# Kernel tuning notes

Measured on AMD Instinct MI355X. Metric: run time of the kernel, lower is better.

Reference implementation:

```python
import jax, jax.numpy as jnp
import numpy as np

B, N, GN, GS = 16, 100000, 4096, 64  # batch, points, num_groups, group_size


def setup_inputs() -> dict:
    key = jax.random.key(0)
    k1, k2, k3 = jax.random.split(key, 3)
    x_proto = jax.random.normal(k1, (B, N, 3), dtype=jnp.float32)
    template = jax.random.normal(k2, (N, 3), dtype=jnp.float32)
    groups = jax.random.randint(k3, (GN, GS), 0, N, dtype=jnp.int32)
    return {"x_proto": x_proto, "template": template, "groups": groups}


def reference(x_proto, template, groups):
    # x_proto: [B, N, 3], template: [N, 3], groups: [GN, GS] int indices
    b, n, _ = x_proto.shape
    Yg = template[groups]                      # [GN, GS, 3] gathered template
    Xg = x_proto[:, groups]                    # [B, GN, GS, 3] gathered current points

    # Kabsch: align template group Y to current X (R @ Y + t ~ X)
    muY = Yg.mean(axis=1)                      # [GN, 3]
    muX = Xg.mean(axis=2)                      # [B, GN, 3]
    Yc = Yg - muY[:, None, :]
    Xc = Xg - muX[:, :, None, :]
    H = jnp.einsum('gni,bgnj->bgij', Yc, Xc)   # [B, GN, 3, 3] covariance
    U, S, Vh = jnp.linalg.svd(H)
    V = jnp.swapaxes(Vh, -2, -1)
    R0 = V @ jnp.swapaxes(U, -2, -1)
    det = jnp.linalg.det(R0)                   # [B, GN]
    # flip last column of V where det < 0 to get a proper rotation
    s = jnp.where(det < 0, -1.0, 1.0).astype(x_proto.dtype)
    col_scale = jnp.stack([jnp.ones_like(s), jnp.ones_like(s), s], axis=-1)  # [B, GN, 3]
    R = (V * col_scale[..., None, :]) @ jnp.swapaxes(U, -2, -1)              # [B, GN, 3, 3]
    t = muX - jnp.einsum('bgij,gj->bgi', R, muY)                             # [B, GN, 3]

    # project template group through (R, t)
    Xg_proj = jnp.einsum('bgij,gnj->bgni', R, Yg) + t[:, :, None, :]         # [B, GN, GS, 3]

    # scatter-add with overlap counting, then average
    flat_idx = groups.reshape(-1)              # [GN*GS]
    out = jnp.zeros_like(x_proto).at[:, flat_idx].add(Xg_proj.reshape(b, -1, 3))
    counts = jnp.zeros((n,), dtype=x_proto.dtype).at[flat_idx].add(1.0)
    counts = jnp.maximum(counts, 1.0)
    return out / counts[None, :, None]
```

## Files before the change

### kernel.cpp

```cpp
#include <hip/hip_runtime.h>
#include <math.h>

static constexpr int BB = 16;
static constexpr int NN = 100000;
static constexpr int GN = 4096;
static constexpr int GS = 64;
static constexpr int NP = BB * GN;
static constexpr int NE = GN * GS;
static constexpr int NBLK = (NN + 255) / 256;

__device__ __forceinline__ float wsum64(float v) {
#pragma unroll
  for (int off = 32; off > 0; off >>= 1) v += __shfl_xor(v, off, 64);
  return v;
}

__global__ __launch_bounds__(256) void k_zero(int4* __restrict__ cnt4) {
  int t = blockIdx.x * 256 + threadIdx.x;
  if (t < NN / 4) cnt4[t] = make_int4(0, 0, 0, 0);
}

__global__ __launch_bounds__(256) void k_tpl(
    const float* __restrict__ tpl, const int* __restrict__ groups,
    float* __restrict__ Yg, float* __restrict__ GmY, int* __restrict__ cnt) {
  int g    = blockIdx.x * 4 + (threadIdx.x >> 6);
  int lane = threadIdx.x & 63;
  int idx = groups[g * GS + lane];
  atomicAdd(&cnt[idx], 1);
  float y0 = tpl[idx * 3 + 0], y1 = tpl[idx * 3 + 1], y2 = tpl[idx * 3 + 2];
  float* o = Yg + ((size_t)g * GS + lane) * 3;
  o[0] = y0; o[1] = y1; o[2] = y2;
  float sy0 = wsum64(y0), sy1 = wsum64(y1), sy2 = wsum64(y2);
  if (lane == 0) {
    const float inv = 1.0f / 64.0f;
    float4 m = make_float4(sy0 * inv, sy1 * inv, sy2 * inv, 0.0f);
    *(float4*)(GmY + (size_t)g * 4) = m;
  }
}

__global__ __launch_bounds__(256) void k_stats(
    const float* __restrict__ x, const float* __restrict__ Yg,
    const float* __restrict__ GmY, const int* __restrict__ groups,
    float* __restrict__ Ht) {
  int wid4 = blockIdx.x * 4 + (threadIdx.x >> 6);
  int lane = threadIdx.x & 63;
  int s    = lane >> 4;
  int l4   = lane & 15;
  int p = wid4 * 4 + s;
  int b = p >> 12;
  int g = p & (GN - 1);

  int4 iv = *(const int4*)(groups + (size_t)g * GS + l4 * 4);
  const float4* yv = (const float4*)(Yg + ((size_t)g * GS + l4 * 4) * 3);
  float4 ya = yv[0], yb = yv[1], yc = yv[2];

  const float* xb = x + (size_t)b * NN * 3;
  float sx0 = 0.f, sx1 = 0.f, sx2 = 0.f;
  float h00 = 0.f, h01 = 0.f, h02 = 0.f;
  float h10 = 0.f, h11 = 0.f, h12 = 0.f;
  float h20 = 0.f, h21 = 0.f, h22 = 0.f;

#define ACC(Y0, Y1, Y2, IDX)                                   \
  {                                                            \
    const float* xp = xb + (size_t)(IDX) * 3;                  \
    float x0 = xp[0], x1 = xp[1], x2 = xp[2];                  \
    sx0 += x0; sx1 += x1; sx2 += x2;                           \
    h00 += (Y0) * x0; h01 += (Y0) * x1; h02 += (Y0) * x2;      \
    h10 += (Y1) * x0; h11 += (Y1) * x1; h12 += (Y1) * x2;      \
    h20 += (Y2) * x0; h21 += (Y2) * x1; h22 += (Y2) * x2;      \
  }
  ACC(ya.x, ya.y, ya.z, iv.x);
  ACC(ya.w, yb.x, yb.y, iv.y);
  ACC(yb.z, yb.w, yc.x, iv.z);
  ACC(yc.y, yc.z, yc.w, iv.w);
#undef ACC

#define RED(V)                                                 \
  V += __shfl_xor(V, 8, 64); V += __shfl_xor(V, 4, 64);        \
  V += __shfl_xor(V, 2, 64); V += __shfl_xor(V, 1, 64);
  RED(sx0) RED(sx1) RED(sx2)
  RED(h00) RED(h01) RED(h02)
  RED(h10) RED(h11) RED(h12)
  RED(h20) RED(h21) RED(h22)
#undef RED

  if (l4 == 0) {
    const float inv = 1.0f / 64.0f;
    float4 m = *(const float4*)(GmY + (size_t)g * 4);
    float mx0 = sx0 * inv, mx1 = sx1 * inv, mx2 = sx2 * inv;
    float4 o0 = make_float4(mx0, mx1, mx2, h00 - m.x * sx0);
    float4 o1 = make_float4(h01 - m.x * sx1, h02 - m.x * sx2,
                            h10 - m.y * sx0, h11 - m.y * sx1);
    float4 o2 = make_float4(h12 - m.y * sx2, h20 - m.z * sx0,
                            h21 - m.z * sx1, h22 - m.z * sx2);
    float* o = Ht + (size_t)p * 12;
    *(float4*)(o + 0) = o0;
    *(float4*)(o + 4) = o1;
    *(float4*)(o + 8) = o2;
  }
}

#define JROT(P, Q, RR)                                                        \
  {                                                                           \
    float apq = K[P][Q];                                                      \
    if (fabsf(apq) > 1e-30f) {                                                \
      float app = K[P][P], aqq = K[Q][Q];                                     \
      float tau = (aqq - app) / (2.0f * apq);                                 \
      float tt = copysignf(1.0f, tau) / (fabsf(tau) + sqrtf(1.0f + tau*tau)); \
      float cc = 1.0f / sqrtf(1.0f + tt * tt);                                \
      float ss = tt * cc;                                                     \
      K[P][P] = app - tt * apq;                                               \
      K[Q][Q] = aqq + tt * apq;                                               \
      K[P][Q] = 0.0f; K[Q][P] = 0.0f;                                         \
      float krp = K[RR][P], krq = K[RR][Q];                                   \
      K[RR][P] = cc * krp - ss * krq; K[P][RR] = K[RR][P];                    \
      K[RR][Q] = ss * krp + cc * krq; K[Q][RR] = K[RR][Q];                    \
      float v0p = V[0][P], v0q = V[0][Q];                                     \
      float v1p = V[1][P], v1q = V[1][Q];                                     \
      float v2p = V[2][P], v2q = V[2][Q];                                     \
      V[0][P] = cc * v0p - ss * v0q; V[0][Q] = ss * v0p + cc * v0q;           \
      V[1][P] = cc * v1p - ss * v1q; V[1][Q] = ss * v1p + cc * v1q;           \
      V[2][P] = cc * v2p - ss * v2q; V[2][Q] = ss * v2p + cc * v2q;           \
    }                                                                         \
  }

#define FIN(AA, BBi, CC)                                                      \
  {                                                                           \
    float va0 = V[0][AA], va1 = V[1][AA], va2 = V[2][AA];                     \
    float vb0 = V[0][BBi], vb1 = V[1][BBi], vb2 = V[2][BBi];                  \
    float vc0 = V[0][CC], vc1 = V[1][CC], vc2 = V[2][CC];                     \
    float ua0 = A[0][0]*va0 + A[0][1]*va1 + A[0][2]*va2;                      \
    float ua1 = A[1][0]*va0 + A[1][1]*va1 + A[1][2]*va2;                      \
    float ua2 = A[2][0]*va0 + A[2][1]*va1 + A[2][2]*va2;                      \
    float il = 1.0f / sqrtf(ua0*ua0 + ua1*ua1 + ua2*ua2 + 1e-30f);            \
    ua0 *= il; ua1 *= il; ua2 *= il;                                          \
    float ub0 = A[0][0]*vb0 + A[0][1]*vb1 + A[0][2]*vb2;                      \
    float ub1 = A[1][0]*vb0 + A[1][1]*vb1 + A[1][2]*vb2;                      \
    float ub2 = A[2][0]*vb0 + A[2][1]*vb1 + A[2][2]*vb2;                      \
    il = 1.0f / sqrtf(ub0*ub0 + ub1*ub1 + ub2*ub2 + 1e-30f);                  \
    ub0 *= il; ub1 *= il; ub2 *= il;                                          \
    float dd = ua0*ub0 + ua1*ub1 + ua2*ub2;                                   \
    ub0 -= dd * ua0; ub1 -= dd * ua1; ub2 -= dd * ua2;                        \
    il = 1.0f / sqrtf(ub0*ub0 + ub1*ub1 + ub2*ub2 + 1e-30f);                  \
    ub0 *= il; ub1 *= il; ub2 *= il;                                          \
    float uc0 = ua1*ub2 - ua2*ub1;                                            \
    float uc1 = ua2*ub0 - ua0*ub2;                                            \
    float uc2 = ua0*ub1 - ua1*ub0;                                            \
    R[0][0] = va0*ua0 + vb0*ub0 + dsg*vc0*uc0;                                \
    R[0][1] = va0*ua1 + vb0*ub1 + dsg*vc0*uc1;                                \
    R[0][2] = va0*ua2 + vb0*ub2 + dsg*vc0*uc2;                                \
    R[1][0] = va1*ua0 + vb1*ub0 + dsg*vc1*uc0;                                \
    R[1][1] = va1*ua1 + vb1*ub1 + dsg*vc1*uc1;                                \
    R[1][2] = va1*ua2 + vb1*ub2 + dsg*vc1*uc2;                                \
    R[2][0] = va2*ua0 + vb2*ub0 + dsg*vc2*uc0;                                \
    R[2][1] = va2*ua1 + vb2*ub1 + dsg*vc2*uc1;                                \
    R[2][2] = va2*ua2 + vb2*ub2 + dsg*vc2*uc2;                                \
  }

__global__ __launch_bounds__(256) void k_svd(
    const float* __restrict__ Ht, const float* __restrict__ GmY,
    float* __restrict__ Rt) {
  int p = blockIdx.x * 256 + threadIdx.x;
  if (p >= NP) return;
  int g = p & (GN - 1);
  const float* h = Ht + (size_t)p * 12;
  float4 f0 = *(const float4*)(h + 0);
  float4 f1 = *(const float4*)(h + 4);
  float4 f2 = *(const float4*)(h + 8);
  float4 m  = *(const float4*)(GmY + (size_t)g * 4);
  float mx0 = f0.x, mx1 = f0.y, mx2 = f0.z;
  float my0 = m.x, my1 = m.y, my2 = m.z;
  float A[3][3];
  A[0][0] = f0.w; A[0][1] = f1.x; A[0][2] = f1.y;
  A[1][0] = f1.z; A[1][1] = f1.w; A[1][2] = f2.x;
  A[2][0] = f2.y; A[2][1] = f2.z; A[2][2] = f2.w;

  float K[3][3];
#pragma unroll
  for (int i = 0; i < 3; ++i)
#pragma unroll
    for (int j = 0; j < 3; ++j)
      K[i][j] = A[0][i]*A[0][j] + A[1][i]*A[1][j] + A[2][i]*A[2][j];

  float V[3][3] = {{1.f,0.f,0.f},{0.f,1.f,0.f},{0.f,0.f,1.f}};
#pragma unroll
  for (int sweep = 0; sweep < 5; ++sweep) {
    JROT(0, 1, 2);
    JROT(0, 2, 1);
    JROT(1, 2, 0);
  }

  float d0 = K[0][0], d1 = K[1][1], d2 = K[2][2];
  float detV = V[0][0]*(V[1][1]*V[2][2] - V[1][2]*V[2][1])
             - V[0][1]*(V[1][0]*V[2][2] - V[1][2]*V[2][0])
             + V[0][2]*(V[1][0]*V[2][1] - V[1][1]*V[2][0]);
  float dsg = (detV < 0.0f) ? -1.0f : 1.0f;

  float R[3][3];
  if (d0 <= d1 && d0 <= d2) {
    FIN(1, 2, 0);
  } else if (d1 <= d0 && d1 <= d2) {
    FIN(2, 0, 1);
  } else {
    FIN(0, 1, 2);
  }

  float t0 = mx0 - (R[0][0]*my0 + R[0][1]*my1 + R[0][2]*my2);
  float t1 = mx1 - (R[1][0]*my0 + R[1][1]*my1 + R[1][2]*my2);
  float t2 = mx2 - (R[2][0]*my0 + R[2][1]*my1 + R[2][2]*my2);

  float* o = Rt + (size_t)p * 12;
  o[0] = R[0][0]; o[1] = R[0][1]; o[2] = R[0][2];
  o[3] = R[1][0]; o[4] = R[1][1]; o[5] = R[1][2];
  o[6] = R[2][0]; o[7] = R[2][1]; o[8] = R[2][2];
  o[9] = t0; o[10] = t1; o[11] = t2;
}

__global__ __launch_bounds__(256) void k_scan1(
    const int* __restrict__ cnt, int* __restrict__ blockSums) {
  __shared__ int lds[4];
  int t = blockIdx.x * 256 + threadIdx.x;
  int v = (t < NN) ? cnt[t] : 0;
#pragma unroll
  for (int off = 32; off > 0; off >>= 1) v += __shfl_xor(v, off, 64);
  if ((threadIdx.x & 63) == 0) lds[threadIdx.x >> 6] = v;
  __syncthreads();
  if (threadIdx.x == 0)
    blockSums[blockIdx.x] = lds[0] + lds[1] + lds[2] + lds[3];
}

__global__ __launch_bounds__(512) void k_scan2(int* __restrict__ blockSums) {
  __shared__ int lds[512];
  int tid = threadIdx.x;
  int v = (tid < NBLK) ? blockSums[tid] : 0;
  lds[tid] = v;
  __syncthreads();
#pragma unroll
  for (int off = 1; off < 512; off <<= 1) {
    int add = (tid >= off) ? lds[tid - off] : 0;
    __syncthreads();
    lds[tid] += add;
    __syncthreads();
  }
  if (tid < NBLK) blockSums[tid] = lds[tid] - v;
}

__global__ __launch_bounds__(256) void k_scan3(
    const int* __restrict__ cnt, const int* __restrict__ blockSums,
    int* __restrict__ row_start, int* __restrict__ cursor) {
  __shared__ int lds[256];
  int tid = threadIdx.x;
  int t = blockIdx.x * 256 + tid;
  int v = (t < NN) ? cnt[t] : 0;
  lds[tid] = v;
  __syncthreads();
#pragma unroll
  for (int off = 1; off < 256; off <<= 1) {
    int add = (tid >= off) ? lds[tid - off] : 0;
    __syncthreads();
    lds[tid] += add;
    __syncthreads();
  }
  if (t < NN) {
    row_start[t] = lds[tid] - v + blockSums[blockIdx.x];
    cursor[t] = 0;
  }
}

__global__ __launch_bounds__(256) void k_fill(
    const int* __restrict__ groups, const int* __restrict__ row_start,
    int* __restrict__ cursor, unsigned* __restrict__ entries) {
  int e = blockIdx.x * 256 + threadIdx.x;
  if (e >= NE) return;
  int n = groups[e];
  int pos = atomicAdd(&cursor[n], 1);
  entries[row_start[n] + pos] = (unsigned)(e >> 6);
}

__global__ __launch_bounds__(256) void k_gather(
    const float* __restrict__ tpl, const int* __restrict__ row_start,
    const int* __restrict__ cnt, const unsigned* __restrict__ entries,
    const float* __restrict__ Rt, float* __restrict__ out) {
  int n = blockIdx.x * 256 + threadIdx.x;
  if (n >= NN) return;
  int b = blockIdx.y;
  int s = row_start[n];
  int c = cnt[n];
  float y0 = tpl[n * 3 + 0], y1 = tpl[n * 3 + 1], y2 = tpl[n * 3 + 2];
  float p0 = 0.f, p1 = 0.f, p2 = 0.f;
  for (int j = 0; j < c; ++j) {
    unsigned g = entries[s + j];
    const float* rt = Rt + ((size_t)b * GN + g) * 12;
    p0 += rt[0] * y0 + rt[1] * y1 + rt[2] * y2 + rt[9];
    p1 += rt[3] * y0 + rt[4] * y1 + rt[5] * y2 + rt[10];
    p2 += rt[6] * y0 + rt[7] * y1 + rt[8] * y2 + rt[11];
  }
  float inv = 1.0f / fmaxf((float)c, 1.0f);
  float* o = out + ((size_t)b * NN + (size_t)n) * 3;
  o[0] = p0 * inv;
  o[1] = p1 * inv;
  o[2] = p2 * inv;
}

extern "C" void kernel_launch(void* const* d_in, const int* in_sizes, int n_in,
                              void* d_out, int out_size, void* d_ws, size_t ws_size,
                              hipStream_t stream) {
  const float* x      = (const float*)d_in[0];
  const float* tpl    = (const float*)d_in[1];
  const int*   groups = (const int*)d_in[2];
  float* out = (float*)d_out;

  char* ws = (char*)d_ws;
  float* Yg        = (float*)ws;
  float* Rt        = (float*)ws;
  float* Ht        = (float*)(ws + (size_t)3 * 1024 * 1024);
  unsigned* entries= (unsigned*)(ws + (size_t)3 * 1024 * 1024);
  int* cursor      = (int*)(ws + (size_t)4 * 1024 * 1024);
  float* GmY       = (float*)(ws + (size_t)6 * 1024 * 1024);
  int* cnt         = (int*)(ws + (size_t)6 * 1024 * 1024 + 65536);
  int* row_start   = (int*)(ws + (size_t)6 * 1024 * 1024 + 65536 + 400000);
  int* blockSums   = (int*)(ws + (size_t)6 * 1024 * 1024 + 65536 + 800000);

  k_zero<<<(NN / 4 + 255) / 256, 256, 0, stream>>>((int4*)cnt);
  k_tpl<<<GN / 4, 256, 0, stream>>>(tpl, groups, Yg, GmY, cnt);
  k_stats<<<NP / 16, 256, 0, stream>>>(x, Yg, GmY, groups, Ht);
  k_svd<<<NP / 256, 256, 0, stream>>>(Ht, GmY, Rt);
  k_scan1<<<NBLK, 256, 0, stream>>>(cnt, blockSums);
  k_scan2<<<1, 512, 0, stream>>>(blockSums);
  k_scan3<<<NBLK, 256, 0, stream>>>(cnt, blockSums, row_start, cursor);
  k_fill<<<NE / 256, 256, 0, stream>>>(groups, row_start, cursor, entries);
  k_gather<<<dim3(NBLK, BB), 256, 0, stream>>>(tpl, row_start, cnt, entries, Rt, out);
}
```

Baseline: 121.1 us.

## Pad x to float4, batch-loop gather, and align Rt to 16 floats

Adds a pre-pass that repacks x into float4-padded points so the stats kernel gathers each point with one vector load, and swizzles the stats block order. Rt is stored at a 16-float stride with vector stores. The gather kernel now handles all batches per point in one thread, reusing the entry list and template reads across batches. In exchange it adds a full extra read/write pass over x and reduces the gather grid to a single batch dimension with many live accumulators.

Result: slower. 149.4 us (+23.3%).

```diff
diff --git a/kernel.cpp b/kernel.cpp
--- a/kernel.cpp
+++ b/kernel.cpp
@@ -15,9 +15,17 @@
   return v;
 }
 
-__global__ __launch_bounds__(256) void k_zero(int4* __restrict__ cnt4) {
+__global__ __launch_bounds__(256) void k_xpad(
+    const float4* __restrict__ x, float4* __restrict__ x4,
+    int4* __restrict__ cnt4) {
   int t = blockIdx.x * 256 + threadIdx.x;
   if (t < NN / 4) cnt4[t] = make_int4(0, 0, 0, 0);
+  if (t >= BB * NN / 4) return;
+  float4 a = x[t * 3 + 0], b = x[t * 3 + 1], c = x[t * 3 + 2];
+  x4[t * 4 + 0] = make_float4(a.x, a.y, a.z, 0.f);
+  x4[t * 4 + 1] = make_float4(a.w, b.x, b.y, 0.f);
+  x4[t * 4 + 2] = make_float4(b.z, b.w, c.x, 0.f);
+  x4[t * 4 + 3] = make_float4(c.y, c.z, c.w, 0.f);
 }
 
 __global__ __launch_bounds__(256) void k_tpl(
@@ -33,16 +41,17 @@
   float sy0 = wsum64(y0), sy1 = wsum64(y1), sy2 = wsum64(y2);
   if (lane == 0) {
     const float inv = 1.0f / 64.0f;
-    float4 m = make_float4(sy0 * inv, sy1 * inv, sy2 * inv, 0.0f);
-    *(float4*)(GmY + (size_t)g * 4) = m;
+    *(float4*)(GmY + (size_t)g * 4) =
+        make_float4(sy0 * inv, sy1 * inv, sy2 * inv, 0.0f);
   }
 }
 
 __global__ __launch_bounds__(256) void k_stats(
-    const float* __restrict__ x, const float* __restrict__ Yg,
+    const float4* __restrict__ x4, const float* __restrict__ Yg,
     const float* __restrict__ GmY, const int* __restrict__ groups,
     float* __restrict__ Ht) {
-  int wid4 = blockIdx.x * 4 + (threadIdx.x >> 6);
+  int bid  = (blockIdx.x & 7) * 512 + (blockIdx.x >> 3);
+  int wid4 = bid * 4 + (threadIdx.x >> 6);
   int lane = threadIdx.x & 63;
   int s    = lane >> 4;
   int l4   = lane & 15;
@@ -54,7 +63,7 @@
   const float4* yv = (const float4*)(Yg + ((size_t)g * GS + l4 * 4) * 3);
   float4 ya = yv[0], yb = yv[1], yc = yv[2];
 
-  const float* xb = x + (size_t)b * NN * 3;
+  const float4* xb4 = x4 + (size_t)b * NN;
   float sx0 = 0.f, sx1 = 0.f, sx2 = 0.f;
   float h00 = 0.f, h01 = 0.f, h02 = 0.f;
   float h10 = 0.f, h11 = 0.f, h12 = 0.f;
@@ -62,12 +71,11 @@
 
 #define ACC(Y0, Y1, Y2, IDX)                                   \
   {                                                            \
-    const float* xp = xb + (size_t)(IDX) * 3;                  \
-    float x0 = xp[0], x1 = xp[1], x2 = xp[2];                  \
-    sx0 += x0; sx1 += x1; sx2 += x2;                           \
-    h00 += (Y0) * x0; h01 += (Y0) * x1; h02 += (Y0) * x2;      \
-    h10 += (Y1) * x0; h11 += (Y1) * x1; h12 += (Y1) * x2;      \
-    h20 += (Y2) * x0; h21 += (Y2) * x1; h22 += (Y2) * x2;      \
+    float4 xv = xb4[IDX];                                      \
+    sx0 += xv.x; sx1 += xv.y; sx2 += xv.z;                     \
+    h00 += (Y0) * xv.x; h01 += (Y0) * xv.y; h02 += (Y0) * xv.z;\
+    h10 += (Y1) * xv.x; h11 += (Y1) * xv.y; h12 += (Y1) * xv.z;\
+    h20 += (Y2) * xv.x; h21 += (Y2) * xv.y; h22 += (Y2) * xv.z;\
   }
   ACC(ya.x, ya.y, ya.z, iv.x);
   ACC(ya.w, yb.x, yb.y, iv.y);
@@ -209,11 +217,10 @@
   float t1 = mx1 - (R[1][0]*my0 + R[1][1]*my1 + R[1][2]*my2);
   float t2 = mx2 - (R[2][0]*my0 + R[2][1]*my1 + R[2][2]*my2);
 
-  float* o = Rt + (size_t)p * 12;
-  o[0] = R[0][0]; o[1] = R[0][1]; o[2] = R[0][2];
-  o[3] = R[1][0]; o[4] = R[1][1]; o[5] = R[1][2];
-  o[6] = R[2][0]; o[7] = R[2][1]; o[8] = R[2][2];
-  o[9] = t0; o[10] = t1; o[11] = t2;
+  float* o = Rt + (size_t)p * 16;
+  *(float4*)(o + 0) = make_float4(R[0][0], R[0][1], R[0][2], R[1][0]);
+  *(float4*)(o + 4) = make_float4(R[1][1], R[1][2], R[2][0], R[2][1]);
+  *(float4*)(o + 8) = make_float4(R[2][2], t0, t1, t2);
 }
 
 __global__ __launch_bounds__(256) void k_scan1(
@@ -269,37 +276,50 @@
 
 __global__ __launch_bounds__(256) void k_fill(
     const int* __restrict__ groups, const int* __restrict__ row_start,
-    int* __restrict__ cursor, unsigned* __restrict__ entries) {
+    int* __restrict__ cursor, int* __restrict__ entries) {
   int e = blockIdx.x * 256 + threadIdx.x;
   if (e >= NE) return;
   int n = groups[e];
   int pos = atomicAdd(&cursor[n], 1);
-  entries[row_start[n] + pos] = (unsigned)(e >> 6);
+  entries[row_start[n] + pos] = e >> 6;
 }
 
 __global__ __launch_bounds__(256) void k_gather(
     const float* __restrict__ tpl, const int* __restrict__ row_start,
-    const int* __restrict__ cnt, const unsigned* __restrict__ entries,
+    const int* __restrict__ cnt, const int* __restrict__ entries,
     const float* __restrict__ Rt, float* __restrict__ out) {
   int n = blockIdx.x * 256 + threadIdx.x;
   if (n >= NN) return;
-  int b = blockIdx.y;
   int s = row_start[n];
   int c = cnt[n];
   float y0 = tpl[n * 3 + 0], y1 = tpl[n * 3 + 1], y2 = tpl[n * 3 + 2];
-  float p0 = 0.f, p1 = 0.f, p2 = 0.f;
+
+  float a0[BB], a1[BB], a2[BB];
+#pragma unroll
+  for (int b = 0; b < BB; ++b) { a0[b] = 0.f; a1[b] = 0.f; a2[b] = 0.f; }
+
   for (int j = 0; j < c; ++j) {
-    unsigned g = entries[s + j];
-    const float* rt = Rt + ((size_t)b * GN + g) * 12;
-    p0 += rt[0] * y0 + rt[1] * y1 + rt[2] * y2 + rt[9];
-    p1 += rt[3] * y0 + rt[4] * y1 + rt[5] * y2 + rt[10];
-    p2 += rt[6] * y0 + rt[7] * y1 + rt[8] * y2 + rt[11];
+    int g = entries[s + j];
+    const float* rg = Rt + (size_t)g * 16;
+#pragma unroll
+    for (int b = 0; b < BB; ++b) {
+      const float* rt = rg + (size_t)b * GN * 16;
+      float4 r0 = *(const float4*)(rt + 0);
+      float4 r1 = *(const float4*)(rt + 4);
+      float4 r2 = *(const float4*)(rt + 8);
+      a0[b] += r0.x * y0 + r0.y * y1 + r0.z * y2 + r2.y;
+      a1[b] += r0.w * y0 + r1.x * y1 + r1.y * y2 + r2.z;
+      a2[b] += r1.z * y0 + r1.w * y1 + r2.x * y2 + r2.w;
+    }
   }
   float inv = 1.0f / fmaxf((float)c, 1.0f);
-  float* o = out + ((size_t)b * NN + (size_t)n) * 3;
-  o[0] = p0 * inv;
-  o[1] = p1 * inv;
-  o[2] = p2 * inv;
+#pragma unroll
+  for (int b = 0; b < BB; ++b) {
+    float* o = out + ((size_t)b * NN + (size_t)n) * 3;
+    o[0] = a0[b] * inv;
+    o[1] = a1[b] * inv;
+    o[2] = a2[b] * inv;
+  }
 }
 
 extern "C" void kernel_launch(void* const* d_in, const int* in_sizes, int n_in,
@@ -311,23 +331,35 @@
   float* out = (float*)d_out;
 
   char* ws = (char*)d_ws;
-  float* Yg        = (float*)ws;
-  float* Rt        = (float*)ws;
-  float* Ht        = (float*)(ws + (size_t)3 * 1024 * 1024);
-  unsigned* entries= (unsigned*)(ws + (size_t)3 * 1024 * 1024);
-  int* cursor      = (int*)(ws + (size_t)4 * 1024 * 1024);
-  float* GmY       = (float*)(ws + (size_t)6 * 1024 * 1024);
-  int* cnt         = (int*)(ws + (size_t)6 * 1024 * 1024 + 65536);
-  int* row_start   = (int*)(ws + (size_t)6 * 1024 * 1024 + 65536 + 400000);
-  int* blockSums   = (int*)(ws + (size_t)6 * 1024 * 1024 + 65536 + 800000);
-
-  k_zero<<<(NN / 4 + 255) / 256, 256, 0, stream>>>((int4*)cnt);
+  size_t o_x4  = 0;
+  size_t o_yg  = o_x4 + 25600000;
+  size_t o_ht  = o_yg + 3145728;
+  size_t o_rt  = o_ht + 3145728;
+  size_t o_gmy = o_rt + 4194304;
+  size_t o_cnt = o_gmy + 65536;
+  size_t o_rs  = o_cnt + 400000;
+  size_t o_cur = o_rs + 400000;
+  size_t o_bs  = o_cur + 400000;
+  size_t o_ent = o_bs + 2048;
+  float* x4        = (float*)(ws + o_x4);
+  float* Yg        = (float*)(ws + o_yg);
+  float* Ht        = (float*)(ws + o_ht);
+  float* Rt        = (float*)(ws + o_rt);
+  float* GmY       = (float*)(ws + o_gmy);
+  int*   cnt       = (int*)(ws + o_cnt);
+  int*   row_start = (int*)(ws + o_rs);
+  int*   cursor    = (int*)(ws + o_cur);
+  int*   blockSums = (int*)(ws + o_bs);
+  int*   entries   = (int*)(ws + o_ent);
+
+  k_xpad<<<(BB * NN / 4 + 255) / 256, 256, 0, stream>>>(
+      (const float4*)x, (float4*)x4, (int4*)cnt);
   k_tpl<<<GN / 4, 256, 0, stream>>>(tpl, groups, Yg, GmY, cnt);
-  k_stats<<<NP / 16, 256, 0, stream>>>(x, Yg, GmY, groups, Ht);
+  k_stats<<<NP / 16, 256, 0, stream>>>((const float4*)x4, Yg, GmY, groups, Ht);
   k_svd<<<NP / 256, 256, 0, stream>>>(Ht, GmY, Rt);
   k_scan1<<<NBLK, 256, 0, stream>>>(cnt, blockSums);
   k_scan2<<<1, 512, 0, stream>>>(blockSums);
   k_scan3<<<NBLK, 256, 0, stream>>>(cnt, blockSums, row_start, cursor);
   k_fill<<<NE / 256, 256, 0, stream>>>(groups, row_start, cursor, entries);
-  k_gather<<<dim3(NBLK, BB), 256, 0, stream>>>(tpl, row_start, cnt, entries, Rt, out);
-}
+  k_gather<<<NBLK, 256, 0, stream>>>(tpl, row_start, cnt, entries, Rt, out);
+}
```
